# Optimization experiments

Measured on AMD Instinct MI355X. Metric: run time of the kernel, lower is better.

Reference implementation:

```python
import itertools
import jax, jax.numpy as jnp
import numpy as np

LATENT_DIM = 8
N = 2 * LATENT_DIM  # width of z_combined = concat([z, dz])
BATCH = 131072

# Static combinatorial index sets, matching the nested-loop order
# (i <= j [<= k]) of the torch implementation exactly.
_PAIRS = np.array(list(itertools.combinations_with_replacement(range(N), 2)), dtype=np.int32)   # [136, 2]
_TRIPLES = np.array(list(itertools.combinations_with_replacement(range(N), 3)), dtype=np.int32)  # [816, 3]


def setup_inputs() -> dict:
    key = jax.random.key(0)
    k1, k2 = jax.random.split(key)
    z = jax.random.normal(k1, (BATCH, LATENT_DIM), dtype=jnp.float32)
    dz = jax.random.normal(k2, (BATCH, LATENT_DIM), dtype=jnp.float32)
    return {"z": z, "dz": dz}


def reference(z, dz):
    # z, dz: [B, latent_dim] -> Theta: [B, 985]
    zc = jnp.concatenate([z, dz], axis=1)  # [B, N]
    B = zc.shape[0]
    ones = jnp.ones((B, 1), dtype=zc.dtype)
    # degree-2 terms: zc[:, i] * zc[:, j] for i <= j, all at once via gather
    deg2 = zc[:, _PAIRS[:, 0]] * zc[:, _PAIRS[:, 1]]  # [B, 136]
    # degree-3 terms: zc[:, i] * zc[:, j] * zc[:, k] for i <= j <= k
    deg3 = zc[:, _TRIPLES[:, 0]] * zc[:, _TRIPLES[:, 1]] * zc[:, _TRIPLES[:, 2]]  # [B, 816]
    sine = jnp.sin(zc)  # [B, N]
    return jnp.concatenate([ones, zc, deg2, deg3, sine], axis=1)  # [B, 985]
```

## Files before the change

### kernel.cpp

```cpp
#include <hip/hip_runtime.h>
#include <cstddef>

#define NCOLS 985
#define RPW   16
#define GSTR  176

__global__ __launch_bounds__(256) void sindy_kernel(const float* __restrict__ z,
                                                    const float* __restrict__ dz,
                                                    float* __restrict__ out, int batch,
                                                    int nwaves) {
  __shared__ unsigned short mtab[1024];
  __shared__ unsigned short ptab[136];
  __shared__ float G[4][GSTR];

  const int tid = threadIdx.x;

  for (int e = tid; e < 1024; e += 256) {
    int a, b;
    if (e < 153)       { a = (e == 0) ? 0 : e; b = 0; }
    else if (e < 969)  {
      int t = e - 153, i = 0;
      for (;;) { int c = (16 - i) * (17 - i) / 2; if (t < c) break; t -= c; ++i; }
      int j = i; while (t >= 16 - j) { t -= 16 - j; ++j; }
      int k = j + t;
      int p = i * 16 - i * (i - 1) / 2 + (j - i);
      a = 17 + p; b = 1 + k;
    }
    else if (e < 985)  { a = 153 + (e - 969); b = 0; }
    else               { a = 169; b = 169; }
    mtab[e] = (unsigned short)(a | (b << 8));
  }
  for (int e = tid; e < 136; e += 256) {
    int p = e, i = 0; while (p >= 16 - i) { p -= 16 - i; ++i; }
    ptab[e] = (unsigned short)(i | ((i + p) << 4));
  }
  __syncthreads();

  const int w = tid >> 6, l = tid & 63;

  unsigned short mt[16];
  #pragma unroll
  for (int wd = 0; wd < 16; ++wd) mt[wd] = mtab[wd * 64 + l];
  const unsigned pe0 = ptab[l];
  const unsigned pe1 = ptab[64 + l];
  const unsigned pe2 = ptab[(128 + l < 136) ? (128 + l) : 135];

  float* Gw = G[w];
  const int gid = blockIdx.x * 4 + w;

  for (int rr = 0; rr < RPW; ++rr) {
    const int row = gid + rr * nwaves;
    if (row >= batch) break;

    float gval = 0.f;
    if (l == 0)       gval = 1.0f;
    else if (l < 9)   gval = z [(size_t)row * 8 + (l - 1)];
    else if (l < 17)  gval = dz[(size_t)row * 8 + (l - 9)];
    const int gaddr = (l < 17) ? l : (152 + l);
    if (l < 24) Gw[gaddr] = gval;

    const float sv = __shfl(gval, l + 1);
    if (l < 16) Gw[153 + l] = __sinf(sv);
    __builtin_amdgcn_sched_barrier(0);

    {
      float a0 = Gw[1 + (pe0 & 15)], b0 = Gw[1 + (pe0 >> 4)];
      Gw[17 + l] = a0 * b0;
      float a1 = Gw[1 + (pe1 & 15)], b1 = Gw[1 + (pe1 >> 4)];
      Gw[17 + 64 + l] = a1 * b1;
      if (l < 8) {
        float a2 = Gw[1 + (pe2 & 15)], b2 = Gw[1 + (pe2 >> 4)];
        Gw[17 + 128 + l] = a2 * b2;
      }
    }
    __builtin_amdgcn_sched_barrier(0);

    float* orow = out + (size_t)row * NCOLS;
    #pragma unroll
    for (int wd = 0; wd < 16; ++wd) {
      const unsigned e = mt[wd];
      const float v = Gw[e & 255] * Gw[e >> 8];
      if (wd < 15)                 orow[wd * 64 + l] = v;
      else if (l < NCOLS - 960)    orow[960 + l] = v;
    }
    __builtin_amdgcn_sched_barrier(0);
  }
}

extern "C" void kernel_launch(void* const* d_in, const int* in_sizes, int n_in,
                              void* d_out, int out_size, void* d_ws, size_t ws_size,
                              hipStream_t stream) {
  const float* z  = (const float*)d_in[0];
  const float* dz = (const float*)d_in[1];
  float* out = (float*)d_out;
  const int batch = in_sizes[0] / 8;

  const int nwaves = (batch + RPW - 1) / RPW;
  const int blocks = (nwaves + 3) / 4;
  sindy_kernel<<<blocks, 256, 0, stream>>>(z, dz, out, batch, nwaves);
}
```

Baseline: 128.8 us.

## Stage 8-row output tiles in LDS and write with float4 stores

```diff
diff --git a/kernel.cpp b/kernel.cpp
--- a/kernel.cpp
+++ b/kernel.cpp
@@ -2,16 +2,19 @@
 #include <cstddef>
 
 #define NCOLS 985
-#define RPW   16
+#define TROWS 8
+#define TILEF (TROWS * NCOLS)
+#define NT4   (TILEF / 4)
 #define GSTR  176
 
 __global__ __launch_bounds__(256) void sindy_kernel(const float* __restrict__ z,
                                                     const float* __restrict__ dz,
                                                     float* __restrict__ out, int batch,
-                                                    int nwaves) {
+                                                    int ntiles) {
   __shared__ unsigned short mtab[1024];
   __shared__ unsigned short ptab[136];
   __shared__ float G[4][GSTR];
+  __shared__ alignas(16) float rowbuf[TILEF];
 
   const int tid = threadIdx.x;
 
@@ -46,44 +49,65 @@
   const unsigned pe2 = ptab[(128 + l < 136) ? (128 + l) : 135];
 
   float* Gw = G[w];
-  const int gid = blockIdx.x * 4 + w;
 
-  for (int rr = 0; rr < RPW; ++rr) {
-    const int row = gid + rr * nwaves;
-    if (row >= batch) break;
+  for (int tile = blockIdx.x; tile < ntiles; tile += gridDim.x) {
+    const int trow0 = tile * TROWS;
+    const int nrows = (batch - trow0 < TROWS) ? (batch - trow0) : TROWS;
 
-    float gval = 0.f;
-    if (l == 0)       gval = 1.0f;
-    else if (l < 9)   gval = z [(size_t)row * 8 + (l - 1)];
-    else if (l < 17)  gval = dz[(size_t)row * 8 + (l - 9)];
-    const int gaddr = (l < 17) ? l : (152 + l);
-    if (l < 24) Gw[gaddr] = gval;
+    #pragma unroll
+    for (int rr = 0; rr < 2; ++rr) {
+      const int lr  = w * 2 + rr;
+      const int row = trow0 + lr;
+      if (row < batch) {
+        float gval = 0.f;
+        if (l == 0)       gval = 1.0f;
+        else if (l < 9)   gval = z [(size_t)row * 8 + (l - 1)];
+        else if (l < 17)  gval = dz[(size_t)row * 8 + (l - 9)];
+        const int gaddr = (l < 17) ? l : (152 + l);
+        if (l < 24) Gw[gaddr] = gval;
 
-    const float sv = __shfl(gval, l + 1);
-    if (l < 16) Gw[153 + l] = __sinf(sv);
-    __builtin_amdgcn_sched_barrier(0);
+        const float sv = __shfl(gval, l + 1);
+        if (l < 16) Gw[153 + l] = __sinf(sv);
+        __builtin_amdgcn_sched_barrier(0);
 
-    {
-      float a0 = Gw[1 + (pe0 & 15)], b0 = Gw[1 + (pe0 >> 4)];
-      Gw[17 + l] = a0 * b0;
-      float a1 = Gw[1 + (pe1 & 15)], b1 = Gw[1 + (pe1 >> 4)];
-      Gw[17 + 64 + l] = a1 * b1;
-      if (l < 8) {
-        float a2 = Gw[1 + (pe2 & 15)], b2 = Gw[1 + (pe2 >> 4)];
-        Gw[17 + 128 + l] = a2 * b2;
+        {
+          float a0 = Gw[1 + (pe0 & 15)], b0 = Gw[1 + (pe0 >> 4)];
+          Gw[17 + l] = a0 * b0;
+          float a1 = Gw[1 + (pe1 & 15)], b1 = Gw[1 + (pe1 >> 4)];
+          Gw[17 + 64 + l] = a1 * b1;
+          if (l < 8) {
+            float a2 = Gw[1 + (pe2 & 15)], b2 = Gw[1 + (pe2 >> 4)];
+            Gw[17 + 128 + l] = a2 * b2;
+          }
+        }
+        __builtin_amdgcn_sched_barrier(0);
+
+        float* rb = rowbuf + lr * NCOLS;
+        #pragma unroll
+        for (int wd = 0; wd < 16; ++wd) {
+          const unsigned e = mt[wd];
+          const float v = Gw[e & 255] * Gw[e >> 8];
+          if (wd < 15)              rb[wd * 64 + l] = v;
+          else if (l < NCOLS - 960) rb[960 + l] = v;
+        }
+        __builtin_amdgcn_sched_barrier(0);
       }
     }
-    __builtin_amdgcn_sched_barrier(0);
+    __syncthreads();
 
-    float* orow = out + (size_t)row * NCOLS;
-    #pragma unroll
-    for (int wd = 0; wd < 16; ++wd) {
-      const unsigned e = mt[wd];
-      const float v = Gw[e & 255] * Gw[e >> 8];
-      if (wd < 15)                 orow[wd * 64 + l] = v;
-      else if (l < NCOLS - 960)    orow[960 + l] = v;
+    if (nrows == TROWS) {
+      float4* __restrict__ dst = (float4*)(out + (size_t)tile * TILEF);
+      const float4* srcq = (const float4*)rowbuf;
+      #pragma unroll 4
+      for (int u = tid; u < NT4; u += 256) {
+        dst[u] = srcq[u];
+      }
+    } else {
+      const int nel = nrows * NCOLS;
+      float* __restrict__ dst = out + (size_t)tile * TILEF;
+      for (int u = tid; u < nel; u += 256) dst[u] = rowbuf[u];
     }
-    __builtin_amdgcn_sched_barrier(0);
+    __syncthreads();
   }
 }
 
@@ -95,7 +119,7 @@
   float* out = (float*)d_out;
   const int batch = in_sizes[0] / 8;
 
-  const int nwaves = (batch + RPW - 1) / RPW;
-  const int blocks = (nwaves + 3) / 4;
-  sindy_kernel<<<blocks, 256, 0, stream>>>(z, dz, out, batch, nwaves);
+  const int ntiles = (batch + TROWS - 1) / TROWS;
+  const int blocks = 2048;
+  sindy_kernel<<<blocks, 256, 0, stream>>>(z, dz, out, batch, ntiles);
 }
```

Result: faster. 113.4 us (-12.0%).
